# Kernel tuning notes

Measured on AMD Instinct MI355X. Metric: run time of the kernel, lower is better.

The kernel has to match this reference:

```python
import jax, jax.numpy as jnp
import numpy as np

B, S, D, H, L, DFF, NA = 128, 52, 1024, 16, 8, 4096, 1000
DK = D // H
KTOP = int((1.0 - 0.9) * S)  # per-row top-k kept before threshold = 5
EPS = 1e-5
SCALE = 1.0 / np.sqrt(DK).astype(np.float32)


def setup_inputs() -> dict:
    key = jax.random.key(0)
    ks = jax.random.split(key, 30)
    # token grid: channels 0,1 in [0,50) so only designated positions match special tokens
    x = jax.random.randint(ks[0], (B, S, 3), 0, 50).astype(jnp.int32)
    act = jax.random.randint(ks[1], (B, S), 0, NA).astype(jnp.int32)
    x = x.at[..., 2].set(act)
    x = x.at[:, 0].set(jnp.array([100, 0, 1], jnp.int32))    # SOS
    x = x.at[:, 26].set(jnp.array([100, 0, 2], jnp.int32))   # SEP
    x = x.at[:, 48:].set(jnp.array([100, 0, 0], jnp.int32))  # PAD tail

    def n(k, shape, scale=0.02):
        return (jax.random.normal(k, shape) * scale).astype(jnp.float32)

    return dict(
        x=x,
        action_emb=n(ks[2], (NA, D), 1.0),
        sep_token=n(ks[3], (D,), 1.0),
        bn_gamma=jnp.ones((S,), jnp.float32),
        bn_beta=jnp.zeros((S,), jnp.float32),
        Wq=n(ks[4], (L, D, D)), bq=jnp.zeros((L, D), jnp.float32),
        Wk=n(ks[5], (L, D, D)), bk=jnp.zeros((L, D), jnp.float32),
        Wv=n(ks[6], (L, D, D)), bv=jnp.zeros((L, D), jnp.float32),
        Wo=n(ks[7], (L, D, D)), bo=jnp.zeros((L, D), jnp.float32),
        W1=n(ks[8], (L, DFF, D)), b1=jnp.zeros((L, DFF), jnp.float32),
        W2=n(ks[9], (L, D, DFF)), b2=jnp.zeros((L, D), jnp.float32),
        ln1_g=jnp.ones((L, D), jnp.float32), ln1_b=jnp.zeros((L, D), jnp.float32),
        ln2_g=jnp.ones((L, D), jnp.float32), ln2_b=jnp.zeros((L, D), jnp.float32),
        Wout=n(ks[10], (3, D)), bout=jnp.zeros((3,), jnp.float32),
    )


def _ln(x, g, b):
    m = x.mean(-1, keepdims=True)
    v = x.var(-1, keepdims=True)
    return (x - m) * jax.lax.rsqrt(v + EPS) * g + b


def reference(x, action_emb, sep_token, bn_gamma, bn_beta,
              Wq, bq, Wk, bk, Wv, bv, Wo, bo,
              W1, b1, W2, b2, ln1_g, ln1_b, ln2_g, ln2_b, Wout, bout):
    PAD = jnp.array([100, 0, 0], x.dtype)
    SEP = jnp.array([100, 0, 2], x.dtype)
    pad = jnp.all(x == PAD, -1)            # [B,S]
    sep = jnp.all(x == SEP, -1)            # [B,S]
    valid = ~pad                            # attend only to non-pad keys

    # token-scatter embedding: sep positions -> sep_token, everything else -> action embedding
    h = jnp.where(sep[..., None], sep_token, action_emb[x[..., 2]])  # [B,S,D]

    # BatchNorm1d(52) over seq-as-channel dim (training-mode batch stats)
    mu = h.mean((0, 2), keepdims=True)
    var = h.var((0, 2), keepdims=True)
    h = (h - mu) * jax.lax.rsqrt(var + EPS) * bn_gamma[None, :, None] + bn_beta[None, :, None]

    for l in range(L):
        q = (h @ Wq[l].T + bq[l]).reshape(B, S, H, DK).transpose(0, 2, 1, 3)
        k = (h @ Wk[l].T + bk[l]).reshape(B, S, H, DK).transpose(0, 2, 1, 3)
        v = (h @ Wv[l].T + bv[l]).reshape(B, S, H, DK).transpose(0, 2, 1, 3)
        scores = jnp.einsum('bhqd,bhkd->bhqk', q, k) * SCALE       # [B,H,S,S]
        scores = jnp.where(valid[:, None, None, :], scores, -1e9)
        thr = jax.lax.top_k(scores, KTOP)[0][..., -1:]              # per-row k-th largest
        sparse = scores * (scores >= thr).astype(scores.dtype)      # zero out sub-threshold
        attn = jax.nn.softmax(sparse, axis=-1)
        o = jnp.einsum('bhqk,bhkd->bhqd', attn, v).transpose(0, 2, 1, 3).reshape(B, S, D)
        o = o @ Wo[l].T + bo[l]
        h = _ln(h + o, ln1_g[l], ln1_b[l])
        f = jax.nn.relu(h @ W1[l].T + b1[l]) @ W2[l].T + b2[l]
        h = _ln(h + f, ln2_g[l], ln2_b[l])

    y = h @ Wout.T + bout                                           # [B,S,3]
    return y[:, -1]
```

## Files before the change

### kernel.cpp

```cpp
#include <hip/hip_runtime.h>
#include <cstddef>
#include <cstdint>

#define B_    128
#define S_    52
#define D_    1024
#define H_    16
#define L_    8
#define DFF_  4096
#define DK_   64
#define T_    (B_*S_)
#define EPS_  1e-5f
#define SCALE_ 0.125f

typedef unsigned short ushortx4 __attribute__((ext_vector_type(4)));
typedef short  bf16x8 __attribute__((ext_vector_type(8)));
typedef float  f32x4  __attribute__((ext_vector_type(4)));

__device__ __forceinline__ unsigned short f2b(float f) {
  unsigned int u = __builtin_bit_cast(unsigned int, f);
  u = u + 0x7fffu + ((u >> 16) & 1u);
  return (unsigned short)(u >> 16);
}
__device__ __forceinline__ float b2f(unsigned short b) {
  unsigned int u = ((unsigned int)b) << 16;
  return __builtin_bit_cast(float, u);
}
__device__ __forceinline__ void gload16(const void* g, void* l) {
  __builtin_amdgcn_global_load_lds((const __attribute__((address_space(1))) unsigned int*)g,
      (__attribute__((address_space(3))) unsigned int*)l, 16, 0, 0);
}

__global__ __launch_bounds__(256) void k_embed(const int* __restrict__ x,
    const float* __restrict__ aemb, const float* __restrict__ sept,
    float* __restrict__ h, float* __restrict__ part, int* __restrict__ mask)
{
  int row = blockIdx.x;
  int b = row / S_;
  int s = row - b * S_;
  const int* xr = x + (size_t)row * 3;
  int x0 = xr[0], x1 = xr[1], x2 = xr[2];
  bool issep = (x0 == 100) && (x1 == 0) && (x2 == 2);
  bool ispad = (x0 == 100) && (x1 == 0) && (x2 == 0);
  int t = threadIdx.x;
  if (t == 0) mask[row] = ispad ? 0 : 1;
  const float* src = issep ? sept : (aemb + (size_t)x2 * D_);
  size_t base = (size_t)row * D_;
  float s1 = 0.f, s2 = 0.f;
#pragma unroll
  for (int i = 0; i < 4; ++i) {
    int d = t + i * 256;
    float v = src[d];
    h[base + d] = v;
    s1 += v;
    s2 += v * v;
  }
#pragma unroll
  for (int off = 32; off; off >>= 1) {
    s1 += __shfl_down(s1, off);
    s2 += __shfl_down(s2, off);
  }
  __shared__ float red[8];
  int lane = t & 63, wid = t >> 6;
  if (lane == 0) { red[wid] = s1; red[4 + wid] = s2; }
  __syncthreads();
  if (t == 0) {
    part[(size_t)s * B_ + b]        = red[0] + red[1] + red[2] + red[3];
    part[(size_t)(S_ + s) * B_ + b] = red[4] + red[5] + red[6] + red[7];
  }
}

__global__ __launch_bounds__(128) void k_bn_reduce(const float* __restrict__ part,
                                                   float* __restrict__ stats)
{
  int s = blockIdx.x;
  int t = threadIdx.x;
  float s1 = part[(size_t)s * B_ + t];
  float s2 = part[(size_t)(S_ + s) * B_ + t];
#pragma unroll
  for (int off = 32; off; off >>= 1) {
    s1 += __shfl_down(s1, off);
    s2 += __shfl_down(s2, off);
  }
  __shared__ float red[4];
  int lane = t & 63, wid = t >> 6;
  if (lane == 0) { red[wid] = s1; red[2 + wid] = s2; }
  __syncthreads();
  if (t == 0) {
    stats[s]      = red[0] + red[1];
    stats[S_ + s] = red[2] + red[3];
  }
}

__global__ __launch_bounds__(256) void k_bn_apply(float* __restrict__ h,
    const float* __restrict__ stats, const float* __restrict__ g,
    const float* __restrict__ bb, unsigned short* __restrict__ hb)
{
  int row = blockIdx.x;
  int s = row % S_;
  const float cnt = (float)(B_ * D_);
  float mu  = stats[s] / cnt;
  float var = stats[S_ + s] / cnt - mu * mu;
  float sc  = rsqrtf(var + EPS_) * g[s];
  float off = bb[s] - mu * sc;
  size_t base = (size_t)row * D_;
  int t = threadIdx.x;
#pragma unroll
  for (int i = 0; i < 4; ++i) {
    int d = t + i * 256;
    float v = h[base + d] * sc + off;
    h[base + d] = v;
    hb[base + d] = f2b(v);
  }
}

__global__ __launch_bounds__(256) void k_wconv(
    const float* __restrict__ wq, const float* __restrict__ wk,
    const float* __restrict__ wv, const float* __restrict__ wo,
    const float* __restrict__ w1, const float* __restrict__ w2,
    unsigned short* __restrict__ out)
{
  const size_t DD = (size_t)D_ * D_;
  const size_t DF = (size_t)DFF_ * D_;
  const size_t total = 4 * DD + 2 * DF;
  size_t stride = (size_t)gridDim.x * 256 * 4;
  for (size_t i = ((size_t)blockIdx.x * 256 + threadIdx.x) * 4; i < total; i += stride) {
    const float* src; size_t off;
    if      (i < DD)          { src = wq; off = i; }
    else if (i < 2 * DD)      { src = wk; off = i - DD; }
    else if (i < 3 * DD)      { src = wv; off = i - 2 * DD; }
    else if (i < 4 * DD)      { src = wo; off = i - 3 * DD; }
    else if (i < 4 * DD + DF) { src = w1; off = i - 4 * DD; }
    else                      { src = w2; off = i - 4 * DD - DF; }
    float4 v = *reinterpret_cast<const float4*>(src + off);
    ushortx4 o = { f2b(v.x), f2b(v.y), f2b(v.z), f2b(v.w) };
    *reinterpret_cast<ushortx4*>(out + i) = o;
  }
}

__global__ __launch_bounds__(256) void k_bcat(const float* __restrict__ bq,
    const float* __restrict__ bk, const float* __restrict__ bv,
    float* __restrict__ out)
{
  int i = blockIdx.x * 256 + threadIdx.x;
  int l = i / 3072, j = i - l * 3072;
  float v = (j < D_) ? bq[l * D_ + j] : (j < 2 * D_) ? bk[l * D_ + j - D_]
                                                     : bv[l * D_ + j - 2 * D_];
  out[i] = v;
}

template<int RELU, int OUTBF16>
__global__ __launch_bounds__(512, 4) void k_gemm8(
    const unsigned short* __restrict__ A, const unsigned short* __restrict__ Wt,
    const float* __restrict__ bias, void* __restrict__ C,
    int Mtiles, int Ntiles, int K, int ldc)
{
  __shared__ unsigned short lds[3 * 12288];
  const int tid = threadIdx.x;
  const int w = tid >> 6, l = tid & 63;

  const int nwg = Mtiles * Ntiles;
  int id = blockIdx.x;
  int swz = (id & 7) * (nwg >> 3) + (id >> 3);
  int bym = swz % Mtiles, bxn = swz / Mtiles;
  const int bm = bym * 256, bn = bxn * 128;

  const int colsw = 16 * ((l & 3) ^ ((l >> 3) & 3));
  const char* gA = (const char*)A + ((size_t)(bm + w * 32 + (l >> 2)) * K) * 2 + colsw;
  const char* gB = (const char*)Wt + ((size_t)(bn + w * 16 + (l >> 2)) * K) * 2 + colsw;
  const size_t r16 = (size_t)16 * K * 2;
  unsigned short* lA = lds + w * 1024;
  unsigned short* lB = lds + 8192 + w * 512;

#define STAGE(tt, bb) do {                          \
    size_t ko_ = (size_t)(tt) * 64;                 \
    unsigned short* la_ = lA + (bb) * 12288;        \
    unsigned short* lb_ = lB + (bb) * 12288;        \
    gload16(gA + ko_,       la_);                   \
    gload16(gA + ko_ + r16, la_ + 512);             \
    gload16(gB + ko_,       lb_);                   \
  } while (0)

  const int fr = l & 15, kg = l >> 4;
  const int wr = w >> 1, wc = w & 1;
  const int xk = 16 * (kg ^ ((fr >> 1) & 3));
  const int aOff = (wr * 64 + fr) * 64 + xk;
  const int bOff = 16384 + (wc * 64 + fr) * 64 + xk;

  f32x4 acc[4][4] = {};
  const int NT = K >> 5;

  STAGE(0, 0);
  STAGE(1, 1);
  int cur = 0;
  for (int t = 0; t < NT; ++t) {
    if (t + 1 < NT) { asm volatile("s_waitcnt vmcnt(3)" ::: "memory"); }
    else            { asm volatile("s_waitcnt vmcnt(0)" ::: "memory"); }
    __builtin_amdgcn_sched_barrier(0);
    __builtin_amdgcn_s_barrier();
    __builtin_amdgcn_sched_barrier(0);
    if (t + 2 < NT) {
      int nb = cur + 2; if (nb >= 3) nb -= 3;
      STAGE(t + 2, nb);
    }
    const char* bp = (const char*)lds + cur * 24576;
    bf16x8 af[4], bfv[4];
#pragma unroll
    for (int mf = 0; mf < 4; ++mf)
      af[mf] = *(const bf16x8*)(bp + aOff + mf * 1024);
#pragma unroll
    for (int nf = 0; nf < 4; ++nf)
      bfv[nf] = *(const bf16x8*)(bp + bOff + nf * 1024);
    asm volatile("s_waitcnt lgkmcnt(0)" ::: "memory");
    __builtin_amdgcn_sched_barrier(0);
    __builtin_amdgcn_s_setprio(1);
#pragma unroll
    for (int mf = 0; mf < 4; ++mf)
#pragma unroll
      for (int nf = 0; nf < 4; ++nf)
        acc[mf][nf] = __builtin_amdgcn_mfma_f32_16x16x32_bf16(af[mf], bfv[nf], acc[mf][nf], 0, 0, 0);
    __builtin_amdgcn_s_setprio(0);
    __builtin_amdgcn_sched_barrier(0);
    cur = (cur == 2) ? 0 : cur + 1;
  }
#undef STAGE

#pragma unroll
  for (int nf = 0; nf < 4; ++nf) {
    int col = bn + wc * 64 + nf * 16 + fr;
    float bv = bias[col];
#pragma unroll
    for (int mf = 0; mf < 4; ++mf) {
      int row0 = bm + wr * 64 + mf * 16 + kg * 4;
#pragma unroll
      for (int j = 0; j < 4; ++j) {
        float v = acc[mf][nf][j] + bv;
        if (RELU) v = fmaxf(v, 0.f);
        if (OUTBF16)
          ((unsigned short*)C)[(size_t)(row0 + j) * ldc + col] = f2b(v);
        else
          ((float*)C)[(size_t)(row0 + j) * ldc + col] = v;
      }
    }
  }
}

__global__ __launch_bounds__(64) void k_attn(const unsigned short* __restrict__ qkv,
    const int* __restrict__ mask, unsigned short* __restrict__ ao)
{
  __shared__ float sc[64][68];
  __shared__ unsigned short ph[64][68];
  __shared__ unsigned short plo[64][68];
  __shared__ unsigned short vT[64][68];
  __shared__ float dnm[64];

  int blk = blockIdx.x;
  int b = blk >> 4, hh = blk & 15;
  int l = threadIdx.x;
  int cl = l & 15, kg = l >> 4;
  const unsigned short* base = qkv + (size_t)(b * S_) * 3072 + hh * 64;

  {
    const unsigned short* vp = base + 2048 + l;
#pragma unroll 4
    for (int k = 0; k < S_; ++k)
      vT[l][k] = vp[(size_t)k * 3072];
#pragma unroll
    for (int k = S_; k < 64; ++k) vT[l][k] = 0;
  }

  bf16x8 qa[4][2], kb[4][2];
#pragma unroll
  for (int mi = 0; mi < 4; ++mi) {
    int row = mi * 16 + cl;
    bool ok = (row < S_);
    const unsigned short* qp = base + (size_t)row * 3072 + kg * 8;
#pragma unroll
    for (int ks = 0; ks < 2; ++ks) {
      bf16x8 z = {};
      qa[mi][ks] = ok ? *reinterpret_cast<const bf16x8*>(qp + ks * 32) : z;
      kb[mi][ks] = ok ? *reinterpret_cast<const bf16x8*>(qp + 1024 + ks * 32) : z;
    }
  }

  f32x4 acc[4][4] = {};
#pragma unroll
  for (int ks = 0; ks < 2; ++ks)
#pragma unroll
    for (int mi = 0; mi < 4; ++mi)
#pragma unroll
      for (int ci = 0; ci < 4; ++ci)
        acc[mi][ci] = __builtin_amdgcn_mfma_f32_16x16x32_bf16(qa[mi][ks], kb[ci][ks], acc[mi][ci], 0, 0, 0);

  int vld[4];
#pragma unroll
  for (int ci = 0; ci < 4; ++ci) {
    int col = ci * 16 + cl;
    vld[ci] = (col < S_) ? mask[b * S_ + col] : 0;
  }
#pragma unroll
  for (int mi = 0; mi < 4; ++mi)
#pragma unroll
    for (int ci = 0; ci < 4; ++ci)
#pragma unroll
      for (int j = 0; j < 4; ++j)
        sc[mi * 16 + kg * 4 + j][ci * 16 + cl] = vld[ci] ? acc[mi][ci][j] * SCALE_ : -1e9f;

  __syncthreads();

  if (l < S_) {
    float v0 = -3e38f, v1 = -3e38f, v2 = -3e38f, v3 = -3e38f, v4 = -3e38f;
    const float4* rp = reinterpret_cast<const float4*>(&sc[l][0]);
#pragma unroll
    for (int c4 = 0; c4 < 13; ++c4) {
      float4 x = rp[c4];
      float xs[4] = { x.x, x.y, x.z, x.w };
#pragma unroll
      for (int u = 0; u < 4; ++u) {
        float xv = xs[u];
        if      (xv > v0) { v4 = v3; v3 = v2; v2 = v1; v1 = v0; v0 = xv; }
        else if (xv > v1) { v4 = v3; v3 = v2; v2 = v1; v1 = xv; }
        else if (xv > v2) { v4 = v3; v3 = v2; v2 = xv; }
        else if (xv > v3) { v4 = v3; v3 = xv; }
        else if (xv > v4) { v4 = xv; }
      }
    }
    float thr = v4;
    float m = fmaxf(v0, 0.f);
    float denom = 0.f;
    for (int c = 0; c < S_; ++c) {
      float xv = sc[l][c];
      float sp = (xv >= thr) ? xv : 0.f;
      float e = __expf(sp - m);
      denom += e;
      unsigned short hi = f2b(e);
      ph[l][c] = hi;
      plo[l][c] = f2b(e - b2f(hi));
    }
#pragma unroll
    for (int c = S_; c < 64; ++c) { ph[l][c] = 0; plo[l][c] = 0; }
    dnm[l] = 1.f / denom;
  }
  __syncthreads();

  f32x4 o[4][4] = {};
#pragma unroll
  for (int ks = 0; ks < 2; ++ks) {
    bf16x8 vf[4];
#pragma unroll
    for (int di = 0; di < 4; ++di)
      vf[di] = *reinterpret_cast<const bf16x8*>(&vT[di * 16 + cl][ks * 32 + kg * 8]);
#pragma unroll
    for (int mi = 0; mi < 4; ++mi) {
      bf16x8 ahi = *reinterpret_cast<const bf16x8*>(&ph[mi * 16 + cl][ks * 32 + kg * 8]);
      bf16x8 alo = *reinterpret_cast<const bf16x8*>(&plo[mi * 16 + cl][ks * 32 + kg * 8]);
#pragma unroll
      for (int di = 0; di < 4; ++di) {
        o[mi][di] = __builtin_amdgcn_mfma_f32_16x16x32_bf16(ahi, vf[di], o[mi][di], 0, 0, 0);
        o[mi][di] = __builtin_amdgcn_mfma_f32_16x16x32_bf16(alo, vf[di], o[mi][di], 0, 0, 0);
      }
    }
  }

#pragma unroll
  for (int mi = 0; mi < 4; ++mi) {
    int row = mi * 16 + kg * 4;
    if (row < S_) {
#pragma unroll
      for (int j = 0; j < 4; ++j) {
        int r = row + j;
        float inv = dnm[r];
        unsigned short* aop = ao + (size_t)(b * S_ + r) * D_ + hh * DK_;
#pragma unroll
        for (int di = 0; di < 4; ++di)
          aop[di * 16 + cl] = f2b(o[mi][di][j] * inv);
      }
    }
  }
}

__global__ __launch_bounds__(256) void k_add_ln(float* __restrict__ h,
    const float* __restrict__ r, const float* __restrict__ g,
    const float* __restrict__ bb, unsigned short* __restrict__ hb)
{
  int row = blockIdx.x;
  size_t base = (size_t)row * D_;
  int t = threadIdx.x;
  float xs[4];
  float s1 = 0.f, s2 = 0.f;
#pragma unroll
  for (int i = 0; i < 4; ++i) {
    int d = t + i * 256;
    float xv = h[base + d] + r[base + d];
    xs[i] = xv;
    s1 += xv;
    s2 += xv * xv;
  }
#pragma unroll
  for (int off = 32; off; off >>= 1) {
    s1 += __shfl_down(s1, off);
    s2 += __shfl_down(s2, off);
  }
  __shared__ float red[8];
  int lane = t & 63, wid = t >> 6;
  if (lane == 0) { red[wid] = s1; red[4 + wid] = s2; }
  __syncthreads();
  if (t == 0) {
    red[0] = red[0] + red[1] + red[2] + red[3];
    red[4] = red[4] + red[5] + red[6] + red[7];
  }
  __syncthreads();
  float mean = red[0] / (float)D_;
  float var  = red[4] / (float)D_ - mean * mean;
  float inv  = rsqrtf(var + EPS_);
#pragma unroll
  for (int i = 0; i < 4; ++i) {
    int d = t + i * 256;
    float v = (xs[i] - mean) * inv * g[d] + bb[d];
    h[base + d] = v;
    hb[base + d] = f2b(v);
  }
}

__global__ __launch_bounds__(256) void k_final(const float* __restrict__ h,
    const float* __restrict__ Wout, const float* __restrict__ bout,
    float* __restrict__ y)
{
  int b = blockIdx.x;
  const float* hr = h + (size_t)(b * S_ + (S_ - 1)) * D_;
  int t = threadIdx.x;
  float p0 = 0.f, p1 = 0.f, p2 = 0.f;
  for (int d = t; d < D_; d += 256) {
    float xv = hr[d];
    p0 += xv * Wout[d];
    p1 += xv * Wout[D_ + d];
    p2 += xv * Wout[2 * D_ + d];
  }
#pragma unroll
  for (int off = 32; off; off >>= 1) {
    p0 += __shfl_down(p0, off);
    p1 += __shfl_down(p1, off);
    p2 += __shfl_down(p2, off);
  }
  __shared__ float red[12];
  int lane = t & 63, wid = t >> 6;
  if (lane == 0) { red[wid] = p0; red[4 + wid] = p1; red[8 + wid] = p2; }
  __syncthreads();
  if (t == 0) {
    y[b * 3 + 0] = red[0] + red[1] + red[2]  + red[3]  + bout[0];
    y[b * 3 + 1] = red[4] + red[5] + red[6]  + red[7]  + bout[1];
    y[b * 3 + 2] = red[8] + red[9] + red[10] + red[11] + bout[2];
  }
}

extern "C" void kernel_launch(void* const* d_in, const int* in_sizes, int n_in,
                              void* d_out, int out_size, void* d_ws, size_t ws_size,
                              hipStream_t stream)
{
  const int*   x    = (const int*)d_in[0];
  const float* aemb = (const float*)d_in[1];
  const float* sept = (const float*)d_in[2];
  const float* bng  = (const float*)d_in[3];
  const float* bnb  = (const float*)d_in[4];
  const float* Wq = (const float*)d_in[5];  const float* bq = (const float*)d_in[6];
  const float* Wk = (const float*)d_in[7];  const float* bk = (const float*)d_in[8];
  const float* Wv = (const float*)d_in[9];  const float* bv = (const float*)d_in[10];
  const float* Wo = (const float*)d_in[11]; const float* bo = (const float*)d_in[12];
  const float* W1 = (const float*)d_in[13]; const float* b1 = (const float*)d_in[14];
  const float* W2 = (const float*)d_in[15]; const float* b2 = (const float*)d_in[16];
  const float* ln1g = (const float*)d_in[17]; const float* ln1b = (const float*)d_in[18];
  const float* ln2g = (const float*)d_in[19]; const float* ln2b = (const float*)d_in[20];
  const float* Wout = (const float*)d_in[21]; const float* bout = (const float*)d_in[22];
  float* out = (float*)d_out;

  float* ws = (float*)d_ws;
  const size_t TD = (size_t)T_ * D_;
  const size_t DD = (size_t)D_ * D_;
  const size_t DF = (size_t)DFF_ * D_;
  float* h   = ws;
  float* tmp = ws + TD;
  unsigned short* hb   = (unsigned short*)(ws + 2 * TD);
  unsigned short* qkvb = (unsigned short*)(ws + 2 * TD + TD / 2);
  unsigned short* aob  = (unsigned short*)(ws + 4 * TD);
  unsigned short* ffb  = (unsigned short*)(ws + 4 * TD + TD / 2);
  unsigned short* wbuf = (unsigned short*)(ws + 6 * TD + TD / 2);
  float* bqkv = ws + 6 * TD + TD / 2 + (4 * DD + 2 * DF) / 2;
  float* stats = bqkv + L_ * 3072;
  float* part  = stats + 2 * S_;
  int*   mask  = (int*)(part + 2 * S_ * B_);

  k_embed<<<T_, 256, 0, stream>>>(x, aemb, sept, h, part, mask);
  k_bn_reduce<<<S_, 128, 0, stream>>>(part, stats);
  k_bn_apply<<<T_, 256, 0, stream>>>(h, stats, bng, bnb, hb);
  k_bcat<<<(L_ * 3072) / 256, 256, 0, stream>>>(bq, bk, bv, bqkv);

  for (int l = 0; l < L_; ++l) {
    k_wconv<<<3072, 256, 0, stream>>>(Wq + l * DD, Wk + l * DD, Wv + l * DD,
                                      Wo + l * DD, W1 + l * DF, W2 + l * DF, wbuf);
    k_gemm8<0, 1><<<26 * 24, 512, 0, stream>>>(hb, wbuf, bqkv + l * 3072,
        qkvb, 26, 24, 1024, 3072);
    k_attn<<<B_ * H_, 64, 0, stream>>>(qkvb, mask, aob);
    k_gemm8<0, 0><<<26 * 8, 512, 0, stream>>>(aob, wbuf + 3 * DD, bo + l * D_,
        tmp, 26, 8, 1024, 1024);
    k_add_ln<<<T_, 256, 0, stream>>>(h, tmp, ln1g + l * D_, ln1b + l * D_, hb);
    k_gemm8<1, 1><<<26 * 32, 512, 0, stream>>>(hb, wbuf + 4 * DD, b1 + l * DFF_,
        ffb, 26, 32, 1024, 4096);
    k_gemm8<0, 0><<<26 * 8, 512, 0, stream>>>(ffb, wbuf + 4 * DD + DF, b2 + l * D_,
        tmp, 26, 8, 4096, 1024);
    k_add_ln<<<T_, 256, 0, stream>>>(h, tmp, ln2g + l * D_, ln2b + l * D_, hb);
  }
  k_final<<<B_, 256, 0, stream>>>(h, Wout, bout, out);
}
```

Measured before the change: 2.587 ms.

## Use persistent atomic tile scheduler and split-K for narrow GEMMs

Turns the GEMM into a persistent kernel that pulls tiles through an atomic counter, launching a fixed grid of 512 or 416 workgroups. The narrow N=1024 output projections (Wo and W2) are split in two along K, and the two partials go to separate buffers. The partials are summed inside add+LayerNorm, with the bias added only by part 0. This is meant to fill the GPU better, since 208 tiles left it under-occupied, at the cost of extra partial-buffer traffic and an atomic per tile. The counters are zeroed once per call and each launch gets its own counter slot. The partial buffers reuse workspace regions (the qkv and ffn buffers), which must not be live at the time they are written.

```diff
diff --git a/kernel.cpp b/kernel.cpp
--- a/kernel.cpp
+++ b/kernel.cpp
@@ -149,28 +149,47 @@
   out[i] = v;
 }
 
+__global__ void k_zero32(int* __restrict__ cnt) { cnt[threadIdx.x] = 0; }
+
 template<int RELU, int OUTBF16>
-__global__ __launch_bounds__(512, 4) void k_gemm8(
+__global__ __launch_bounds__(512, 4) void k_gemm_p(
     const unsigned short* __restrict__ A, const unsigned short* __restrict__ Wt,
-    const float* __restrict__ bias, void* __restrict__ C,
-    int Mtiles, int Ntiles, int K, int ldc)
+    const float* __restrict__ bias, void* __restrict__ C0, void* __restrict__ C1,
+    int Mtiles, int Ntiles, int parts, int K, int ldc, int* __restrict__ cnt)
 {
   __shared__ unsigned short lds[3 * 12288];
+  __shared__ int sTile;
   const int tid = threadIdx.x;
   const int w = tid >> 6, l = tid & 63;
 
-  const int nwg = Mtiles * Ntiles;
-  int id = blockIdx.x;
-  int swz = (id & 7) * (nwg >> 3) + (id >> 3);
-  int bym = swz % Mtiles, bxn = swz / Mtiles;
-  const int bm = bym * 256, bn = bxn * 128;
+  const int tpp = Mtiles * Ntiles;
+  const int nwg = tpp * parts;
+  const int KH = K / parts;
+  const int NT = KH >> 5;
 
   const int colsw = 16 * ((l & 3) ^ ((l >> 3) & 3));
-  const char* gA = (const char*)A + ((size_t)(bm + w * 32 + (l >> 2)) * K) * 2 + colsw;
-  const char* gB = (const char*)Wt + ((size_t)(bn + w * 16 + (l >> 2)) * K) * 2 + colsw;
   const size_t r16 = (size_t)16 * K * 2;
   unsigned short* lA = lds + w * 1024;
   unsigned short* lB = lds + 8192 + w * 512;
+  const int fr = l & 15, kg = l >> 4;
+  const int wr = w >> 1, wc = w & 1;
+  const int xk = 16 * (kg ^ ((fr >> 1) & 3));
+  const int aOff = (wr * 64 + fr) * 64 + xk;
+  const int bOff = 16384 + (wc * 64 + fr) * 64 + xk;
+
+  for (;;) {
+    if (tid == 0) sTile = atomicAdd(cnt, 1);
+    __syncthreads();
+    const int tl = sTile;
+    if (tl >= nwg) break;
+    const int part = tl / tpp;
+    const int rem  = tl - part * tpp;
+    const int bxn  = rem % Ntiles;
+    const int bym  = rem / Ntiles;
+    const int bm = bym * 256, bn = bxn * 128;
+
+    const char* gA = (const char*)A + ((size_t)(bm + w * 32 + (l >> 2)) * K + (size_t)part * KH) * 2 + colsw;
+    const char* gB = (const char*)Wt + ((size_t)(bn + w * 16 + (l >> 2)) * K + (size_t)part * KH) * 2 + colsw;
 
 #define STAGE(tt, bb) do {                          \
     size_t ko_ = (size_t)(tt) * 64;                 \
@@ -181,65 +200,59 @@
     gload16(gB + ko_,       lb_);                   \
   } while (0)
 
-  const int fr = l & 15, kg = l >> 4;
-  const int wr = w >> 1, wc = w & 1;
-  const int xk = 16 * (kg ^ ((fr >> 1) & 3));
-  const int aOff = (wr * 64 + fr) * 64 + xk;
-  const int bOff = 16384 + (wc * 64 + fr) * 64 + xk;
-
-  f32x4 acc[4][4] = {};
-  const int NT = K >> 5;
-
-  STAGE(0, 0);
-  STAGE(1, 1);
-  int cur = 0;
-  for (int t = 0; t < NT; ++t) {
-    if (t + 1 < NT) { asm volatile("s_waitcnt vmcnt(3)" ::: "memory"); }
-    else            { asm volatile("s_waitcnt vmcnt(0)" ::: "memory"); }
-    __builtin_amdgcn_sched_barrier(0);
-    __builtin_amdgcn_s_barrier();
-    __builtin_amdgcn_sched_barrier(0);
-    if (t + 2 < NT) {
-      int nb = cur + 2; if (nb >= 3) nb -= 3;
-      STAGE(t + 2, nb);
-    }
-    const char* bp = (const char*)lds + cur * 24576;
-    bf16x8 af[4], bfv[4];
-#pragma unroll
-    for (int mf = 0; mf < 4; ++mf)
-      af[mf] = *(const bf16x8*)(bp + aOff + mf * 1024);
-#pragma unroll
-    for (int nf = 0; nf < 4; ++nf)
-      bfv[nf] = *(const bf16x8*)(bp + bOff + nf * 1024);
-    asm volatile("s_waitcnt lgkmcnt(0)" ::: "memory");
-    __builtin_amdgcn_sched_barrier(0);
-    __builtin_amdgcn_s_setprio(1);
-#pragma unroll
-    for (int mf = 0; mf < 4; ++mf)
+    f32x4 acc[4][4] = {};
+    STAGE(0, 0);
+    STAGE(1, 1);
+    int cur = 0;
+    for (int t = 0; t < NT; ++t) {
+      if (t + 1 < NT) { asm volatile("s_waitcnt vmcnt(3)" ::: "memory"); }
+      else            { asm volatile("s_waitcnt vmcnt(0)" ::: "memory"); }
+      __builtin_amdgcn_sched_barrier(0);
+      __builtin_amdgcn_s_barrier();
+      __builtin_amdgcn_sched_barrier(0);
+      if (t + 2 < NT) {
+        int nb = cur + 2; if (nb >= 3) nb -= 3;
+        STAGE(t + 2, nb);
+      }
+      const char* bp = (const char*)lds + cur * 24576;
+      bf16x8 af[4], bfv[4];
+#pragma unroll
+      for (int mf = 0; mf < 4; ++mf)
+        af[mf] = *(const bf16x8*)(bp + aOff + mf * 1024);
 #pragma unroll
       for (int nf = 0; nf < 4; ++nf)
-        acc[mf][nf] = __builtin_amdgcn_mfma_f32_16x16x32_bf16(af[mf], bfv[nf], acc[mf][nf], 0, 0, 0);
-    __builtin_amdgcn_s_setprio(0);
-    __builtin_amdgcn_sched_barrier(0);
-    cur = (cur == 2) ? 0 : cur + 1;
-  }
+        bfv[nf] = *(const bf16x8*)(bp + bOff + nf * 1024);
+      asm volatile("s_waitcnt lgkmcnt(0)" ::: "memory");
+      __builtin_amdgcn_sched_barrier(0);
+      __builtin_amdgcn_s_setprio(1);
+#pragma unroll
+      for (int mf = 0; mf < 4; ++mf)
+#pragma unroll
+        for (int nf = 0; nf < 4; ++nf)
+          acc[mf][nf] = __builtin_amdgcn_mfma_f32_16x16x32_bf16(af[mf], bfv[nf], acc[mf][nf], 0, 0, 0);
+      __builtin_amdgcn_s_setprio(0);
+      __builtin_amdgcn_sched_barrier(0);
+      cur = (cur == 2) ? 0 : cur + 1;
+    }
 #undef STAGE
 
-#pragma unroll
-  for (int nf = 0; nf < 4; ++nf) {
-    int col = bn + wc * 64 + nf * 16 + fr;
-    float bv = bias[col];
-#pragma unroll
-    for (int mf = 0; mf < 4; ++mf) {
-      int row0 = bm + wr * 64 + mf * 16 + kg * 4;
-#pragma unroll
-      for (int j = 0; j < 4; ++j) {
-        float v = acc[mf][nf][j] + bv;
-        if (RELU) v = fmaxf(v, 0.f);
-        if (OUTBF16)
-          ((unsigned short*)C)[(size_t)(row0 + j) * ldc + col] = f2b(v);
-        else
-          ((float*)C)[(size_t)(row0 + j) * ldc + col] = v;
+    void* C = part ? C1 : C0;
+#pragma unroll
+    for (int nf = 0; nf < 4; ++nf) {
+      int col = bn + wc * 64 + nf * 16 + fr;
+      float bv = (part == 0) ? bias[col] : 0.f;
+#pragma unroll
+      for (int mf = 0; mf < 4; ++mf) {
+        int row0 = bm + wr * 64 + mf * 16 + kg * 4;
+#pragma unroll
+        for (int j = 0; j < 4; ++j) {
+          float v = acc[mf][nf][j] + bv;
+          if (RELU) v = fmaxf(v, 0.f);
+          if (OUTBF16)
+            ((unsigned short*)C)[(size_t)(row0 + j) * ldc + col] = f2b(v);
+          else
+            ((float*)C)[(size_t)(row0 + j) * ldc + col] = v;
+        }
       }
     }
   }
@@ -380,8 +393,9 @@
 }
 
 __global__ __launch_bounds__(256) void k_add_ln(float* __restrict__ h,
-    const float* __restrict__ r, const float* __restrict__ g,
-    const float* __restrict__ bb, unsigned short* __restrict__ hb)
+    const float* __restrict__ r0, const float* __restrict__ r1,
+    const float* __restrict__ g, const float* __restrict__ bb,
+    unsigned short* __restrict__ hb)
 {
   int row = blockIdx.x;
   size_t base = (size_t)row * D_;
@@ -391,7 +405,7 @@
 #pragma unroll
   for (int i = 0; i < 4; ++i) {
     int d = t + i * 256;
-    float xv = h[base + d] + r[base + d];
+    float xv = h[base + d] + r0[base + d] + r1[base + d];
     xs[i] = xv;
     s1 += xv;
     s2 += xv * xv;
@@ -484,11 +498,15 @@
   unsigned short* aob  = (unsigned short*)(ws + 4 * TD);
   unsigned short* ffb  = (unsigned short*)(ws + 4 * TD + TD / 2);
   unsigned short* wbuf = (unsigned short*)(ws + 6 * TD + TD / 2);
+  float* Pff = ws + 4 * TD + TD / 2;
+  float* Pqk = ws + 2 * TD + TD / 2;
   float* bqkv = ws + 6 * TD + TD / 2 + (4 * DD + 2 * DF) / 2;
   float* stats = bqkv + L_ * 3072;
   float* part  = stats + 2 * S_;
   int*   mask  = (int*)(part + 2 * S_ * B_);
-
+  int*   cnt   = mask + T_;
+
+  k_zero32<<<1, 32, 0, stream>>>(cnt);
   k_embed<<<T_, 256, 0, stream>>>(x, aemb, sept, h, part, mask);
   k_bn_reduce<<<S_, 128, 0, stream>>>(part, stats);
   k_bn_apply<<<T_, 256, 0, stream>>>(h, stats, bng, bnb, hb);
@@ -497,17 +515,17 @@
   for (int l = 0; l < L_; ++l) {
     k_wconv<<<3072, 256, 0, stream>>>(Wq + l * DD, Wk + l * DD, Wv + l * DD,
                                       Wo + l * DD, W1 + l * DF, W2 + l * DF, wbuf);
-    k_gemm8<0, 1><<<26 * 24, 512, 0, stream>>>(hb, wbuf, bqkv + l * 3072,
-        qkvb, 26, 24, 1024, 3072);
+    k_gemm_p<0, 1><<<512, 512, 0, stream>>>(hb, wbuf, bqkv + l * 3072,
+        qkvb, qkvb, 26, 24, 1, 1024, 3072, cnt + l * 4 + 0);
     k_attn<<<B_ * H_, 64, 0, stream>>>(qkvb, mask, aob);
-    k_gemm8<0, 0><<<26 * 8, 512, 0, stream>>>(aob, wbuf + 3 * DD, bo + l * D_,
-        tmp, 26, 8, 1024, 1024);
-    k_add_ln<<<T_, 256, 0, stream>>>(h, tmp, ln1g + l * D_, ln1b + l * D_, hb);
-    k_gemm8<1, 1><<<26 * 32, 512, 0, stream>>>(hb, wbuf + 4 * DD, b1 + l * DFF_,
-        ffb, 26, 32, 1024, 4096);
-    k_gemm8<0, 0><<<26 * 8, 512, 0, stream>>>(ffb, wbuf + 4 * DD + DF, b2 + l * D_,
-        tmp, 26, 8, 4096, 1024);
-    k_add_ln<<<T_, 256, 0, stream>>>(h, tmp, ln2g + l * D_, ln2b + l * D_, hb);
+    k_gemm_p<0, 0><<<416, 512, 0, stream>>>(aob, wbuf + 3 * DD, bo + l * D_,
+        tmp, Pff, 26, 8, 2, 1024, 1024, cnt + l * 4 + 1);
+    k_add_ln<<<T_, 256, 0, stream>>>(h, tmp, Pff, ln1g + l * D_, ln1b + l * D_, hb);
+    k_gemm_p<1, 1><<<512, 512, 0, stream>>>(hb, wbuf + 4 * DD, b1 + l * DFF_,
+        ffb, ffb, 26, 32, 1, 1024, 4096, cnt + l * 4 + 2);
+    k_gemm_p<0, 0><<<416, 512, 0, stream>>>(ffb, wbuf + 4 * DD + DF, b2 + l * D_,
+        tmp, Pqk, 26, 8, 2, 4096, 1024, cnt + l * 4 + 3);
+    k_add_ln<<<T_, 256, 0, stream>>>(h, tmp, Pqk, ln2g + l * D_, ln2b + l * D_, hb);
   }
   k_final<<<B_, 256, 0, stream>>>(h, Wout, bout, out);
 }
```

After: 2.771 ms. 7.1% more time.

## Convert all layer weights to bf16 in one launch and group-swizzle GEMM tiles

Applied to the files above, without the earlier changes.

Weight conversion from fp32 to bf16 for all eight layers now runs in a single kernel before the layer loop, provided the workspace is large enough. This removes eight separate conversion launches and the serial dependency each one put in front of a layer's GEMMs. The GEMM tile mapping also changes to a grouped 8x8 swizzle so that neighbouring workgroups share A and B tiles in L2. Both changes cost extra workspace memory and a fallback path for when the workspace is too small.

```diff
diff --git a/kernel.cpp b/kernel.cpp
--- a/kernel.cpp
+++ b/kernel.cpp
@@ -114,24 +114,27 @@
   }
 }
 
-__global__ __launch_bounds__(256) void k_wconv(
-    const float* __restrict__ wq, const float* __restrict__ wk,
-    const float* __restrict__ wv, const float* __restrict__ wo,
-    const float* __restrict__ w1, const float* __restrict__ w2,
-    unsigned short* __restrict__ out)
+__global__ __launch_bounds__(256) void k_wconv8(
+    const float* __restrict__ Wq, const float* __restrict__ Wk,
+    const float* __restrict__ Wv, const float* __restrict__ Wo,
+    const float* __restrict__ W1, const float* __restrict__ W2,
+    unsigned short* __restrict__ out, int nlayers)
 {
   const size_t DD = (size_t)D_ * D_;
   const size_t DF = (size_t)DFF_ * D_;
-  const size_t total = 4 * DD + 2 * DF;
+  const size_t per = 4 * DD + 2 * DF;
+  const size_t total = per * (size_t)nlayers;
   size_t stride = (size_t)gridDim.x * 256 * 4;
   for (size_t i = ((size_t)blockIdx.x * 256 + threadIdx.x) * 4; i < total; i += stride) {
+    size_t lay = i / per;
+    size_t j = i - lay * per;
     const float* src; size_t off;
-    if      (i < DD)          { src = wq; off = i; }
-    else if (i < 2 * DD)      { src = wk; off = i - DD; }
-    else if (i < 3 * DD)      { src = wv; off = i - 2 * DD; }
-    else if (i < 4 * DD)      { src = wo; off = i - 3 * DD; }
-    else if (i < 4 * DD + DF) { src = w1; off = i - 4 * DD; }
-    else                      { src = w2; off = i - 4 * DD - DF; }
+    if      (j < DD)          { src = Wq + lay * DD; off = j; }
+    else if (j < 2 * DD)      { src = Wk + lay * DD; off = j - DD; }
+    else if (j < 3 * DD)      { src = Wv + lay * DD; off = j - 2 * DD; }
+    else if (j < 4 * DD)      { src = Wo + lay * DD; off = j - 3 * DD; }
+    else if (j < 4 * DD + DF) { src = W1 + lay * DF; off = j - 4 * DD; }
+    else                      { src = W2 + lay * DF; off = j - 4 * DD - DF; }
     float4 v = *reinterpret_cast<const float4*>(src + off);
     ushortx4 o = { f2b(v.x), f2b(v.y), f2b(v.z), f2b(v.w) };
     *reinterpret_cast<ushortx4*>(out + i) = o;
@@ -162,7 +165,13 @@
   const int nwg = Mtiles * Ntiles;
   int id = blockIdx.x;
   int swz = (id & 7) * (nwg >> 3) + (id >> 3);
-  int bym = swz % Mtiles, bxn = swz / Mtiles;
+  const int stripe = swz / (Ntiles << 3);
+  const int r = swz - stripe * (Ntiles << 3);
+  int hg = Mtiles - (stripe << 3); if (hg > 8) hg = 8;
+  const int c = r / (hg << 3);
+  const int q = r - c * (hg << 3);
+  const int bym = (stripe << 3) + (q >> 3);
+  const int bxn = (c << 3) + (q & 7);
   const int bm = bym * 256, bn = bxn * 128;
 
   const int colsw = 16 * ((l & 3) ^ ((l >> 3) & 3));
@@ -477,35 +486,42 @@
   const size_t TD = (size_t)T_ * D_;
   const size_t DD = (size_t)D_ * D_;
   const size_t DF = (size_t)DFF_ * D_;
+  const size_t WPL = 4 * DD + 2 * DF;
   float* h   = ws;
   float* tmp = ws + TD;
   unsigned short* hb   = (unsigned short*)(ws + 2 * TD);
   unsigned short* qkvb = (unsigned short*)(ws + 2 * TD + TD / 2);
   unsigned short* aob  = (unsigned short*)(ws + 4 * TD);
   unsigned short* ffb  = (unsigned short*)(ws + 4 * TD + TD / 2);
-  unsigned short* wbuf = (unsigned short*)(ws + 6 * TD + TD / 2);
-  float* bqkv = ws + 6 * TD + TD / 2 + (4 * DD + 2 * DF) / 2;
+  float* bqkv  = ws + 6 * TD + TD / 2;
   float* stats = bqkv + L_ * 3072;
   float* part  = stats + 2 * S_;
   int*   mask  = (int*)(part + 2 * S_ * B_);
+  size_t usedB = ((char*)(mask + T_) - (char*)ws + 255) & ~(size_t)255;
+  unsigned short* wbuf = (unsigned short*)((char*)ws + usedB);
+  const int all8 = (ws_size >= usedB + 8 * WPL * sizeof(unsigned short)) ? 1 : 0;
 
   k_embed<<<T_, 256, 0, stream>>>(x, aemb, sept, h, part, mask);
   k_bn_reduce<<<S_, 128, 0, stream>>>(part, stats);
   k_bn_apply<<<T_, 256, 0, stream>>>(h, stats, bng, bnb, hb);
   k_bcat<<<(L_ * 3072) / 256, 256, 0, stream>>>(bq, bk, bv, bqkv);
+  if (all8)
+    k_wconv8<<<4096, 256, 0, stream>>>(Wq, Wk, Wv, Wo, W1, W2, wbuf, L_);
 
   for (int l = 0; l < L_; ++l) {
-    k_wconv<<<3072, 256, 0, stream>>>(Wq + l * DD, Wk + l * DD, Wv + l * DD,
-                                      Wo + l * DD, W1 + l * DF, W2 + l * DF, wbuf);
-    k_gemm8<0, 1><<<26 * 24, 512, 0, stream>>>(hb, wbuf, bqkv + l * 3072,
+    unsigned short* wl = all8 ? (wbuf + (size_t)l * WPL) : wbuf;
+    if (!all8)
+      k_wconv8<<<3072, 256, 0, stream>>>(Wq + l * DD, Wk + l * DD, Wv + l * DD,
+                                         Wo + l * DD, W1 + l * DF, W2 + l * DF, wbuf, 1);
+    k_gemm8<0, 1><<<26 * 24, 512, 0, stream>>>(hb, wl, bqkv + l * 3072,
         qkvb, 26, 24, 1024, 3072);
     k_attn<<<B_ * H_, 64, 0, stream>>>(qkvb, mask, aob);
-    k_gemm8<0, 0><<<26 * 8, 512, 0, stream>>>(aob, wbuf + 3 * DD, bo + l * D_,
+    k_gemm8<0, 0><<<26 * 8, 512, 0, stream>>>(aob, wl + 3 * DD, bo + l * D_,
         tmp, 26, 8, 1024, 1024);
     k_add_ln<<<T_, 256, 0, stream>>>(h, tmp, ln1g + l * D_, ln1b + l * D_, hb);
-    k_gemm8<1, 1><<<26 * 32, 512, 0, stream>>>(hb, wbuf + 4 * DD, b1 + l * DFF_,
+    k_gemm8<1, 1><<<26 * 32, 512, 0, stream>>>(hb, wl + 4 * DD, b1 + l * DFF_,
         ffb, 26, 32, 1024, 4096);
-    k_gemm8<0, 0><<<26 * 8, 512, 0, stream>>>(ffb, wbuf + 4 * DD + DF, b2 + l * D_,
+    k_gemm8<0, 0><<<26 * 8, 512, 0, stream>>>(ffb, wl + 4 * DD + DF, b2 + l * D_,
         tmp, 26, 8, 4096, 1024);
     k_add_ln<<<T_, 256, 0, stream>>>(h, tmp, ln2g + l * D_, ln2b + l * D_, hb);
   }
```

New measurement: 2.438 ms. 1.06x faster.
